# Kernel tuning notes

Hardware: AMD Instinct MI355X
Metric: run time of the kernel (lower is better)

The kernel has to match this reference:

```python
import jax, jax.numpy as jnp
import numpy as np

D_MODEL = 2048
NUM_HEADS = 16
HEAD_DIM = D_MODEL // NUM_HEADS
B, T = 2, 2048


def setup_inputs() -> dict:
    key = jax.random.key(0)
    ks = jax.random.split(key, 6)
    x = jax.random.normal(ks[0], (B, T, D_MODEL), dtype=jnp.float32)
    # RoPE tables: angles theta_i = 10000^(-2i/d), half-dim tables [T, HEAD_DIM//2]
    pos = jnp.arange(T, dtype=jnp.float32)[:, None]
    inv_freq = 1.0 / (10000.0 ** (jnp.arange(0, HEAD_DIM, 2, dtype=jnp.float32) / HEAD_DIM))
    ang = pos * inv_freq[None, :]
    sin = jnp.sin(ang)
    cos = jnp.cos(ang)
    doc_ids = jnp.sort(jax.random.randint(ks[1], (B, T), 0, 4), axis=-1).astype(jnp.int32)
    W_qkv = jax.random.normal(ks[2], (D_MODEL, D_MODEL + 2 * HEAD_DIM), dtype=jnp.float32) * 0.02
    W_out = jax.random.normal(ks[3], (D_MODEL, D_MODEL), dtype=jnp.float32) * 0.02
    return {"x": x, "sin": sin, "cos": cos, "doc_ids": doc_ids, "W_qkv": W_qkv, "W_out": W_out}


def _apply_rope(x, sin, cos):
    # x: [..., T, ..., HEAD_DIM]; sin/cos: [T, HEAD_DIM//2], broadcast to x's rank
    if x.ndim == 4:  # [B, T, H, D]
        s, c = sin[None, :, None, :], cos[None, :, None, :]
    else:  # [B, T, D]
        s, c = sin[None, :, :], cos[None, :, :]
    x1, x2 = jnp.split(x, 2, axis=-1)
    return jnp.concatenate([x1 * c - x2 * s, x2 * c + x1 * s], axis=-1)


def reference(x, sin, cos, doc_ids, W_qkv, W_out):
    b, t, _ = x.shape
    qkv = x @ W_qkv  # [B, T, D_MODEL + 2*HEAD_DIM]
    q = qkv[..., :D_MODEL].reshape(b, t, NUM_HEADS, HEAD_DIM)
    k = qkv[..., D_MODEL:D_MODEL + HEAD_DIM]  # [B, T, HEAD_DIM] single KV head
    v = qkv[..., D_MODEL + HEAD_DIM:]         # [B, T, HEAD_DIM]
    q = _apply_rope(q, sin, cos)
    k = _apply_rope(k, sin, cos)
    # doc-packed causal mask -> additive bias [B, 1, T, T]
    neg_inf = jnp.finfo(q.dtype).min / 2
    causal = jnp.tril(jnp.ones((t, t), dtype=jnp.bool_))
    same_doc = doc_ids[:, :, None] == doc_ids[:, None, :]
    mask = (causal[None, :, :] & same_doc)[:, None, :, :]
    bias = jnp.where(mask, jnp.array(0.0, q.dtype), neg_inf)
    scale = 1.0 / jnp.sqrt(jnp.array(HEAD_DIM, q.dtype))
    scores = jnp.einsum("bthd,bsd->bhts", q, k) * scale + bias  # [B, H, T, T]
    attn = jax.nn.softmax(scores, axis=-1)
    out = jnp.einsum("bhts,bsd->bthd", attn, v).reshape(b, t, D_MODEL)
    return out @ W_out
```

## Files before the change

kernel.cpp:

```cpp
#include <hip/hip_runtime.h>
#include <math.h>

#define D_MODEL 2048
#define NUM_HEADS 16
#define HEAD_DIM 128
#define BB 2
#define TT 2048
#define QKV_N 2304
#define KOFF 2048
#define VOFF 2176

typedef __attribute__((ext_vector_type(8))) short short8;
typedef __attribute__((ext_vector_type(4))) float f32x4;

static __device__ __forceinline__ short f2bf(float f) {
  union { float f; unsigned u; } x; x.f = f;
  unsigned r = (x.u + 0x7FFFu + ((x.u >> 16) & 1u)) >> 16;
  return (short)r;
}

#define GLD16(gp, lp)                                              \
  __builtin_amdgcn_global_load_lds(                                \
      (const __attribute__((address_space(1))) void*)(gp),         \
      (__attribute__((address_space(3))) void*)(lp), 16, 0, 0)

static __device__ __forceinline__ void swizzle_xy(int& bx, int& by) {
  const int gx = gridDim.x;
  const int lin = blockIdx.y * gx + blockIdx.x;
  const int band = lin / (gx * 8);
  const int rem = lin - band * gx * 8;
  by = band * 8 + (rem & 7);
  bx = rem >> 3;
}

__global__ __launch_bounds__(256) void gemm_qkv_rope(
    const short* __restrict__ A, const short* __restrict__ Bt,
    short* __restrict__ qkv, short* __restrict__ Vtb,
    const float* __restrict__ sin_t, const float* __restrict__ cos_t)
{
  __shared__ short As[2 * 128 * 32];
  __shared__ short Bs[2 * 128 * 32];
  const int K = D_MODEL;

  int bx, by;
  swizzle_xy(bx, by);

  const int tid = threadIdx.x;
  const int w = tid >> 6, l = tid & 63;
  const int quad = l >> 4, l16 = l & 15;
  const int wm = w >> 1, wn = w & 1;
  const int m0 = by * 128, n0 = bx * 128;

  f32x4 acc[4][4];
#pragma unroll
  for (int i = 0; i < 4; i++)
#pragma unroll
    for (int j = 0; j < 4; j++) acc[i][j] = (f32x4){0.f, 0.f, 0.f, 0.f};

  const int cswz = ((l & 3) ^ ((l >> 3) & 3)) * 8;
  const short* aA = A + (size_t)(m0 + w * 32 + (l >> 2)) * K + cswz;
  const short* aB = Bt + (size_t)(n0 + w * 32 + (l >> 2)) * K + cswz;
  short* lA = As + w * 1024;
  short* lB = Bs + w * 1024;

  const int aswz = (quad ^ ((l16 >> 1) & 3)) * 8;
  const short* Ard = As + (size_t)(wm * 64 + l16) * 32 + aswz;
  const short* Brd = Bs + (size_t)(wn * 16 + l16) * 32 + aswz;

  for (int k0 = 0; k0 < K; k0 += 64) {
    __syncthreads();
#pragma unroll
    for (int h = 0; h < 2; h++) {
      const int go = k0 + h * 32;
      const int lo = h * 4096;
      GLD16(aA + go, lA + lo);
      GLD16(aA + go + (size_t)16 * K, lA + lo + 512);
      GLD16(aB + go, lB + lo);
      GLD16(aB + go + (size_t)16 * K, lB + lo + 512);
    }
    __syncthreads();

#pragma unroll
    for (int kc = 0; kc < 2; kc++) {
      short8 af[4], bf[4];
#pragma unroll
      for (int mi = 0; mi < 4; mi++)
        af[mi] = *(const short8*)(Ard + kc * 4096 + mi * 512);
#pragma unroll
      for (int ni = 0; ni < 4; ni++)
        bf[ni] = *(const short8*)(Brd + kc * 4096 + ni * 1024);
#pragma unroll
      for (int mi = 0; mi < 4; mi++)
#pragma unroll
        for (int ni = 0; ni < 4; ni++)
          acc[mi][ni] =
              __builtin_amdgcn_mfma_f32_16x16x32_bf16(af[mi], bf[ni], acc[mi][ni], 0, 0, 0);
    }
  }

  const int colbase = wn * 16 + l16;
  const bool is_v = (n0 == VOFF);

#pragma unroll
  for (int mi = 0; mi < 4; mi++) {
#pragma unroll
    for (int r = 0; r < 4; r++) {
      const int row = m0 + wm * 64 + mi * 16 + quad * 4 + r;
      const int b = row >> 11, t = row & (TT - 1);
#pragma unroll
      for (int ni = 0; ni < 2; ni++) {
        const int cloc = ni * 32 + colbase;
        const float c1 = acc[mi][ni][r];
        const float c2 = acc[mi][ni + 2][r];
        if (!is_v) {
          const float sn = sin_t[t * 64 + cloc];
          const float cs = cos_t[t * 64 + cloc];
          short* op = qkv + (size_t)row * QKV_N + n0 + cloc;
          op[0]  = f2bf(c1 * cs - c2 * sn);
          op[64] = f2bf(c2 * cs + c1 * sn);
        } else {
          Vtb[((size_t)(b * 128 + cloc) << 11) + t]      = f2bf(c1);
          Vtb[((size_t)(b * 128 + cloc + 64) << 11) + t] = f2bf(c2);
        }
      }
    }
  }
}

__global__ __launch_bounds__(256) void gemm_mfma_bt(
    const short* __restrict__ A, const short* __restrict__ Bt,
    float* __restrict__ C, int M, int N, int K)
{
  __shared__ short As[2 * 128 * 32];
  __shared__ short Bs[2 * 128 * 32];

  int bx, by;
  swizzle_xy(bx, by);

  const int tid = threadIdx.x;
  const int w = tid >> 6, l = tid & 63;
  const int quad = l >> 4, l16 = l & 15;
  const int wm = w >> 1, wn = w & 1;
  const int m0 = by * 128, n0 = bx * 128;

  f32x4 acc[4][4];
#pragma unroll
  for (int i = 0; i < 4; i++)
#pragma unroll
    for (int j = 0; j < 4; j++) acc[i][j] = (f32x4){0.f, 0.f, 0.f, 0.f};

  const int cswz = ((l & 3) ^ ((l >> 3) & 3)) * 8;
  const short* aA = A + (size_t)(m0 + w * 32 + (l >> 2)) * K + cswz;
  const short* aB = Bt + (size_t)(n0 + w * 32 + (l >> 2)) * K + cswz;
  short* lA = As + w * 1024;
  short* lB = Bs + w * 1024;

  const int aswz = (quad ^ ((l16 >> 1) & 3)) * 8;
  const short* Ard = As + (size_t)(wm * 64 + l16) * 32 + aswz;
  const short* Brd = Bs + (size_t)(wn * 64 + l16) * 32 + aswz;

  for (int k0 = 0; k0 < K; k0 += 64) {
    __syncthreads();
#pragma unroll
    for (int h = 0; h < 2; h++) {
      const int go = k0 + h * 32;
      const int lo = h * 4096;
      GLD16(aA + go, lA + lo);
      GLD16(aA + go + (size_t)16 * K, lA + lo + 512);
      GLD16(aB + go, lB + lo);
      GLD16(aB + go + (size_t)16 * K, lB + lo + 512);
    }
    __syncthreads();

#pragma unroll
    for (int kc = 0; kc < 2; kc++) {
      short8 af[4], bf[4];
#pragma unroll
      for (int mi = 0; mi < 4; mi++)
        af[mi] = *(const short8*)(Ard + kc * 4096 + mi * 512);
#pragma unroll
      for (int ni = 0; ni < 4; ni++)
        bf[ni] = *(const short8*)(Brd + kc * 4096 + ni * 512);
#pragma unroll
      for (int mi = 0; mi < 4; mi++)
#pragma unroll
        for (int ni = 0; ni < 4; ni++)
          acc[mi][ni] =
              __builtin_amdgcn_mfma_f32_16x16x32_bf16(af[mi], bf[ni], acc[mi][ni], 0, 0, 0);
    }
  }

#pragma unroll
  for (int mi = 0; mi < 4; mi++) {
#pragma unroll
    for (int ni = 0; ni < 4; ni++) {
#pragma unroll
      for (int r = 0; r < 4; r++) {
        const int row = m0 + wm * 64 + mi * 16 + quad * 4 + r;
        const int col = n0 + wn * 64 + ni * 16 + l16;
        C[(size_t)row * N + col] = acc[mi][ni][r];
      }
    }
  }
}

#define XB_BLOCKS 8192
#define WQ_BLOCKS (72 * 64)
#define WO_BLOCKS (64 * 64)

__global__ __launch_bounds__(256) void prep_all(
    const float* __restrict__ x, short* __restrict__ xb,
    const float* __restrict__ Wq, short* __restrict__ Wqt,
    const float* __restrict__ Wo, short* __restrict__ Wot)
{
  const int bid = blockIdx.x;
  const int tid = threadIdx.x;

  if (bid < XB_BLOCKS) {
    const size_t i4 = (size_t)bid * 256 + tid;
    float4 v = *(const float4*)(x + i4 * 4);
    short4 o;
    o.x = f2bf(v.x); o.y = f2bf(v.y); o.z = f2bf(v.z); o.w = f2bf(v.w);
    *(short4*)(xb + i4 * 4) = o;
    return;
  }

  __shared__ float t[32][33];
  const float* W;
  short* Wt;
  int N, tile, ntx;
  if (bid < XB_BLOCKS + WQ_BLOCKS) {
    tile = bid - XB_BLOCKS; W = Wq; Wt = Wqt; N = QKV_N; ntx = 72;
  } else {
    tile = bid - XB_BLOCKS - WQ_BLOCKS; W = Wo; Wt = Wot; N = D_MODEL; ntx = 64;
  }
  const int K = D_MODEL;
  const int bx = tile % ntx, byy = tile / ntx;
  const int tx = tid & 31, ty = tid >> 5;
  const int n0 = bx * 32, k0 = byy * 32;
#pragma unroll
  for (int j = 0; j < 4; j++)
    t[ty + j * 8][tx] = W[(size_t)(k0 + ty + j * 8) * N + n0 + tx];
  __syncthreads();
#pragma unroll
  for (int j = 0; j < 4; j++)
    Wt[(size_t)(n0 + ty + j * 8) * K + k0 + tx] = f2bf(t[tx][ty + j * 8]);
}

#define PSTR 72

__global__ __launch_bounds__(256) void attn_mfma(
    const short* __restrict__ qkv, const short* __restrict__ Vtb,
    const int* __restrict__ doc_ids, short* __restrict__ attn_out)
{
  __shared__ short Ks[64 * 128];
  __shared__ short Vt[128 * 64];
  __shared__ short Pbuf[4 * 16 * PSTR];
  __shared__ int doc_s[64];

  const int qt = blockIdx.x, h = blockIdx.y, b = blockIdx.z;
  const int q0 = qt * 64;
  const int tid = threadIdx.x;
  const int w = tid >> 6;
  const int lane = tid & 63;
  const int quad = lane >> 4, l16 = lane & 15;

  const short* qp = qkv + (size_t)(b * TT + q0 + w * 16 + l16) * QKV_N
                    + h * HEAD_DIM + quad * 8;
  short8 Qf[4];
#pragma unroll
  for (int kc = 0; kc < 4; kc++) Qf[kc] = *(const short8*)(qp + kc * 32);

  const int docmin_q = doc_ids[b * TT + q0];
  const int docmax_q = doc_ids[b * TT + q0 + 63];

  int qg[4], mydoc[4];
  float l_i[4];
#pragma unroll
  for (int r = 0; r < 4; r++) {
    qg[r] = q0 + w * 16 + quad * 4 + r;
    mydoc[r] = doc_ids[b * TT + qg[r]];
    l_i[r] = 0.f;
  }
  f32x4 O[8];
#pragma unroll
  for (int v8 = 0; v8 < 8; v8++) O[v8] = (f32x4){0.f, 0.f, 0.f, 0.f};

  short* Pw = Pbuf + w * 16 * PSTR;
  const float scale = 0.08838834764831844f;

  const int x7 = l16 & 7;
  int kcol[4], vcol[2];
#pragma unroll
  for (int kc = 0; kc < 4; kc++) kcol[kc] = ((kc * 4 + quad) ^ x7) * 8;
#pragma unroll
  for (int ks = 0; ks < 2; ks++) vcol[ks] = ((ks * 4 + quad) ^ x7) * 8;

  for (int st = 0; st <= qt; st++) {
    const int s0 = st * 64;
    const int dmin_s = doc_ids[b * TT + s0];
    const int dmax_s = doc_ids[b * TT + s0 + 63];
    if (dmax_s < docmin_q) continue;
    const bool full = (st < qt) && (dmin_s == docmax_q);

    __syncthreads();
#pragma unroll
    for (int j = 0; j < 4; j++) {
      const int f = w * 4 + j;
      const int rg = f * 4 + (lane >> 4);
      GLD16(qkv + (size_t)(b * TT + s0 + rg) * QKV_N + KOFF
                + (((lane & 15) ^ (rg & 7)) * 8),
            Ks + f * 512);
    }
#pragma unroll
    for (int j = 0; j < 4; j++) {
      const int f = w * 4 + j;
      const int n = f * 8 + (lane >> 3);
      GLD16(Vtb + (((size_t)(b * 128 + n)) << 11) + s0
                + (((lane & 7) ^ (lane >> 3)) * 8),
            Vt + f * 512);
    }
    if (!full && tid < 64) doc_s[tid] = doc_ids[b * TT + s0 + tid];
    __syncthreads();

    f32x4 S[4];
#pragma unroll
    for (int ns = 0; ns < 4; ns++) {
      f32x4 acc = (f32x4){0.f, 0.f, 0.f, 0.f};
      const short* krow = Ks + (ns * 16 + l16) * 128;
#pragma unroll
      for (int kc = 0; kc < 4; kc++) {
        short8 kf = *(const short8*)(krow + kcol[kc]);
        acc = __builtin_amdgcn_mfma_f32_16x16x32_bf16(Qf[kc], kf, acc, 0, 0, 0);
      }
      S[ns] = acc;
    }

    if (full) {
#pragma unroll
      for (int ns = 0; ns < 4; ns++)
#pragma unroll
        for (int r = 0; r < 4; r++) {
          const float p = __expf(S[ns][r] * scale);
          l_i[r] += p;
          Pw[(quad * 4 + r) * PSTR + ns * 16 + l16] = f2bf(p);
        }
    } else {
#pragma unroll
      for (int ns = 0; ns < 4; ns++) {
        const int s_loc = ns * 16 + l16;
        const int sg = s0 + s_loc;
        const int sdoc = doc_s[s_loc];
#pragma unroll
        for (int r = 0; r < 4; r++) {
          const bool ok = (sg <= qg[r]) && (sdoc == mydoc[r]);
          const float p = ok ? __expf(S[ns][r] * scale) : 0.f;
          l_i[r] += p;
          Pw[(quad * 4 + r) * PSTR + ns * 16 + l16] = f2bf(p);
        }
      }
    }

#pragma unroll
    for (int ks = 0; ks < 2; ks++) {
      short8 pf = *(const short8*)(Pw + l16 * PSTR + ks * 32 + quad * 8);
#pragma unroll
      for (int v8 = 0; v8 < 8; v8++) {
        short8 vf = *(const short8*)(Vt + (v8 * 16 + l16) * 64 + vcol[ks]);
        O[v8] = __builtin_amdgcn_mfma_f32_16x16x32_bf16(pf, vf, O[v8], 0, 0, 0);
      }
    }
  }

#pragma unroll
  for (int off = 8; off >= 1; off >>= 1)
#pragma unroll
    for (int r = 0; r < 4; r++) l_i[r] += __shfl_xor(l_i[r], off);

#pragma unroll
  for (int r = 0; r < 4; r++) {
    const float inv = 1.f / l_i[r];
    short* op = attn_out + (size_t)(b * TT + qg[r]) * D_MODEL + h * HEAD_DIM + l16;
#pragma unroll
    for (int v8 = 0; v8 < 8; v8++)
      op[v8 * 16] = f2bf(O[v8][r] * inv);
  }
}

extern "C" void kernel_launch(void* const* d_in, const int* in_sizes, int n_in,
                              void* d_out, int out_size, void* d_ws, size_t ws_size,
                              hipStream_t stream)
{
  const float* x     = (const float*)d_in[0];
  const float* sin_t = (const float*)d_in[1];
  const float* cos_t = (const float*)d_in[2];
  const int*   doc   = (const int*)  d_in[3];
  const float* W_qkv = (const float*)d_in[4];
  const float* W_out = (const float*)d_in[5];
  float* out = (float*)d_out;

  const int M = BB * TT;

  char* p = (char*)d_ws;
  short* qkv_bf = (short*)p; p += (size_t)M * QKV_N * 2;
  short* xb     = (short*)p; p += (size_t)M * D_MODEL * 2;
  short* attn_bf = xb;
  short* Vtb    = (short*)p; p += (size_t)BB * 128 * TT * 2;
  short* Wqkv_t = (short*)p; p += (size_t)QKV_N * D_MODEL * 2;
  short* Wout_t = (short*)p;

  prep_all<<<XB_BLOCKS + WQ_BLOCKS + WO_BLOCKS, 256, 0, stream>>>(
      x, xb, W_qkv, Wqkv_t, W_out, Wout_t);

  {
    dim3 grid(QKV_N / 128, M / 128);
    gemm_qkv_rope<<<grid, 256, 0, stream>>>(xb, Wqkv_t, qkv_bf, Vtb, sin_t, cos_t);
  }
  {
    dim3 grid(TT / 64, NUM_HEADS, BB);
    attn_mfma<<<grid, 256, 0, stream>>>(qkv_bf, Vtb, doc, attn_bf);
  }
  {
    dim3 grid(D_MODEL / 128, M / 128);
    gemm_mfma_bt<<<grid, 256, 0, stream>>>(attn_bf, Wout_t, out, M, D_MODEL, D_MODEL);
  }
}
```

Before: 267.8 us.

## Process two attention heads per block to reuse shared K/V tiles

Each attention block now handles two query heads, so the single shared KV head's K and V tiles loaded into LDS are reused twice per load. The grid is halved along the head dimension, and per-thread registers for Q fragments, O accumulators and row sums double. It also sets launch_bounds(256,2) to cap register use. The risks are higher register pressure or spills, and fewer blocks in flight, which can hurt load balance across the causal triangle.

```diff
diff --git a/kernel.cpp b/kernel.cpp
--- a/kernel.cpp
+++ b/kernel.cpp
@@ -249,7 +249,7 @@
 
 #define PSTR 72
 
-__global__ __launch_bounds__(256) void attn_mfma(
+__global__ __launch_bounds__(256, 2) void attn_mfma(
     const short* __restrict__ qkv, const short* __restrict__ Vtb,
     const int* __restrict__ doc_ids, short* __restrict__ attn_out)
 {
@@ -258,33 +258,40 @@
   __shared__ short Pbuf[4 * 16 * PSTR];
   __shared__ int doc_s[64];
 
-  const int qt = blockIdx.x, h = blockIdx.y, b = blockIdx.z;
+  const int qt = blockIdx.x, h0 = blockIdx.y * 2, b = blockIdx.z;
   const int q0 = qt * 64;
   const int tid = threadIdx.x;
   const int w = tid >> 6;
   const int lane = tid & 63;
   const int quad = lane >> 4, l16 = lane & 15;
 
-  const short* qp = qkv + (size_t)(b * TT + q0 + w * 16 + l16) * QKV_N
-                    + h * HEAD_DIM + quad * 8;
-  short8 Qf[4];
-#pragma unroll
-  for (int kc = 0; kc < 4; kc++) Qf[kc] = *(const short8*)(qp + kc * 32);
+  short8 Qf[2][4];
+#pragma unroll
+  for (int hh = 0; hh < 2; hh++) {
+    const short* qp = qkv + (size_t)(b * TT + q0 + w * 16 + l16) * QKV_N
+                      + (h0 + hh) * HEAD_DIM + quad * 8;
+#pragma unroll
+    for (int kc = 0; kc < 4; kc++) Qf[hh][kc] = *(const short8*)(qp + kc * 32);
+  }
 
   const int docmin_q = doc_ids[b * TT + q0];
   const int docmax_q = doc_ids[b * TT + q0 + 63];
 
   int qg[4], mydoc[4];
-  float l_i[4];
 #pragma unroll
   for (int r = 0; r < 4; r++) {
     qg[r] = q0 + w * 16 + quad * 4 + r;
     mydoc[r] = doc_ids[b * TT + qg[r]];
-    l_i[r] = 0.f;
-  }
-  f32x4 O[8];
-#pragma unroll
-  for (int v8 = 0; v8 < 8; v8++) O[v8] = (f32x4){0.f, 0.f, 0.f, 0.f};
+  }
+  float l_i[2][4];
+  f32x4 O[2][8];
+#pragma unroll
+  for (int hh = 0; hh < 2; hh++) {
+#pragma unroll
+    for (int r = 0; r < 4; r++) l_i[hh][r] = 0.f;
+#pragma unroll
+    for (int v8 = 0; v8 < 8; v8++) O[hh][v8] = (f32x4){0.f, 0.f, 0.f, 0.f};
+  }
 
   short* Pw = Pbuf + w * 16 * PSTR;
   const float scale = 0.08838834764831844f;
@@ -323,67 +330,74 @@
     if (!full && tid < 64) doc_s[tid] = doc_ids[b * TT + s0 + tid];
     __syncthreads();
 
-    f32x4 S[4];
-#pragma unroll
-    for (int ns = 0; ns < 4; ns++) {
-      f32x4 acc = (f32x4){0.f, 0.f, 0.f, 0.f};
-      const short* krow = Ks + (ns * 16 + l16) * 128;
-#pragma unroll
-      for (int kc = 0; kc < 4; kc++) {
-        short8 kf = *(const short8*)(krow + kcol[kc]);
-        acc = __builtin_amdgcn_mfma_f32_16x16x32_bf16(Qf[kc], kf, acc, 0, 0, 0);
+#pragma unroll
+    for (int hh = 0; hh < 2; hh++) {
+      f32x4 S[4];
+#pragma unroll
+      for (int ns = 0; ns < 4; ns++) {
+        f32x4 acc = (f32x4){0.f, 0.f, 0.f, 0.f};
+        const short* krow = Ks + (ns * 16 + l16) * 128;
+#pragma unroll
+        for (int kc = 0; kc < 4; kc++) {
+          short8 kf = *(const short8*)(krow + kcol[kc]);
+          acc = __builtin_amdgcn_mfma_f32_16x16x32_bf16(Qf[hh][kc], kf, acc, 0, 0, 0);
+        }
+        S[ns] = acc;
       }
-      S[ns] = acc;
-    }
-
-    if (full) {
-#pragma unroll
-      for (int ns = 0; ns < 4; ns++)
-#pragma unroll
-        for (int r = 0; r < 4; r++) {
-          const float p = __expf(S[ns][r] * scale);
-          l_i[r] += p;
-          Pw[(quad * 4 + r) * PSTR + ns * 16 + l16] = f2bf(p);
-        }
-    } else {
-#pragma unroll
-      for (int ns = 0; ns < 4; ns++) {
-        const int s_loc = ns * 16 + l16;
-        const int sg = s0 + s_loc;
-        const int sdoc = doc_s[s_loc];
-#pragma unroll
-        for (int r = 0; r < 4; r++) {
-          const bool ok = (sg <= qg[r]) && (sdoc == mydoc[r]);
-          const float p = ok ? __expf(S[ns][r] * scale) : 0.f;
-          l_i[r] += p;
-          Pw[(quad * 4 + r) * PSTR + ns * 16 + l16] = f2bf(p);
+
+      if (full) {
+#pragma unroll
+        for (int ns = 0; ns < 4; ns++)
+#pragma unroll
+          for (int r = 0; r < 4; r++) {
+            const float p = __expf(S[ns][r] * scale);
+            l_i[hh][r] += p;
+            Pw[(quad * 4 + r) * PSTR + ns * 16 + l16] = f2bf(p);
+          }
+      } else {
+#pragma unroll
+        for (int ns = 0; ns < 4; ns++) {
+          const int s_loc = ns * 16 + l16;
+          const int sg = s0 + s_loc;
+          const int sdoc = doc_s[s_loc];
+#pragma unroll
+          for (int r = 0; r < 4; r++) {
+            const bool ok = (sg <= qg[r]) && (sdoc == mydoc[r]);
+            const float p = ok ? __expf(S[ns][r] * scale) : 0.f;
+            l_i[hh][r] += p;
+            Pw[(quad * 4 + r) * PSTR + ns * 16 + l16] = f2bf(p);
+          }
         }
       }
-    }
-
-#pragma unroll
-    for (int ks = 0; ks < 2; ks++) {
-      short8 pf = *(const short8*)(Pw + l16 * PSTR + ks * 32 + quad * 8);
-#pragma unroll
-      for (int v8 = 0; v8 < 8; v8++) {
-        short8 vf = *(const short8*)(Vt + (v8 * 16 + l16) * 64 + vcol[ks]);
-        O[v8] = __builtin_amdgcn_mfma_f32_16x16x32_bf16(pf, vf, O[v8], 0, 0, 0);
+
+#pragma unroll
+      for (int ks = 0; ks < 2; ks++) {
+        short8 pf = *(const short8*)(Pw + l16 * PSTR + ks * 32 + quad * 8);
+#pragma unroll
+        for (int v8 = 0; v8 < 8; v8++) {
+          short8 vf = *(const short8*)(Vt + (v8 * 16 + l16) * 64 + vcol[ks]);
+          O[hh][v8] = __builtin_amdgcn_mfma_f32_16x16x32_bf16(pf, vf, O[hh][v8], 0, 0, 0);
+        }
       }
     }
   }
 
 #pragma unroll
-  for (int off = 8; off >= 1; off >>= 1)
-#pragma unroll
-    for (int r = 0; r < 4; r++) l_i[r] += __shfl_xor(l_i[r], off);
-
-#pragma unroll
-  for (int r = 0; r < 4; r++) {
-    const float inv = 1.f / l_i[r];
-    short* op = attn_out + (size_t)(b * TT + qg[r]) * D_MODEL + h * HEAD_DIM + l16;
-#pragma unroll
-    for (int v8 = 0; v8 < 8; v8++)
-      op[v8 * 16] = f2bf(O[v8][r] * inv);
+  for (int hh = 0; hh < 2; hh++) {
+#pragma unroll
+    for (int off = 8; off >= 1; off >>= 1)
+#pragma unroll
+      for (int r = 0; r < 4; r++) l_i[hh][r] += __shfl_xor(l_i[hh][r], off);
+
+#pragma unroll
+    for (int r = 0; r < 4; r++) {
+      const float inv = 1.f / l_i[hh][r];
+      short* op = attn_out + (size_t)(b * TT + qg[r]) * D_MODEL
+                  + (h0 + hh) * HEAD_DIM + l16;
+#pragma unroll
+      for (int v8 = 0; v8 < 8; v8++)
+        op[v8 * 16] = f2bf(O[hh][v8][r] * inv);
+    }
   }
 }
 
@@ -417,7 +431,7 @@
     gemm_qkv_rope<<<grid, 256, 0, stream>>>(xb, Wqkv_t, qkv_bf, Vtb, sin_t, cos_t);
   }
   {
-    dim3 grid(TT / 64, NUM_HEADS, BB);
+    dim3 grid(TT / 64, NUM_HEADS / 2, BB);
     attn_mfma<<<grid, 256, 0, stream>>>(qkv_bf, Vtb, doc, attn_bf);
   }
   {
```

Result: slower. 273.4 us (+2.1%).
